# Kernel tuning notes

Measured on AMD Instinct MI355X. Metric: run time of the kernel, lower is better.

## Reference

```python
import jax, jax.numpy as jnp
import numpy as np

L, H, HS, D, T, V, B = 6, 6, 64, 384, 256, 65, 64
EPS = 1e-5


def layer_norm(x, g, b):
    m = x.mean(-1, keepdims=True)
    v = x.var(-1, keepdims=True)
    return (x - m) / jnp.sqrt(v + EPS) * g + b


def setup_inputs() -> dict:
    key = jax.random.key(0)
    ks = jax.random.split(key, 12)
    s = 0.02
    return {
        "idx": jax.random.randint(ks[0], (B, T), 0, V),
        "targets": jax.random.randint(ks[1], (B, T), 0, V),
        "tok_emb": s * jax.random.normal(ks[2], (V, D), jnp.float32),
        "pos_emb": s * jax.random.normal(ks[3], (T, D), jnp.float32),
        "Wq": s * jax.random.normal(ks[4], (L, H, D, HS), jnp.float32),
        "Wk": s * jax.random.normal(ks[5], (L, H, D, HS), jnp.float32),
        "Wv": s * jax.random.normal(ks[6], (L, H, D, HS), jnp.float32),
        "Wproj": s * jax.random.normal(ks[7], (L, D, D), jnp.float32),
        "bproj": jnp.zeros((L, D), jnp.float32),
        "W1": s * jax.random.normal(ks[8], (L, D, 4 * D), jnp.float32),
        "b1": jnp.zeros((L, 4 * D), jnp.float32),
        "W2": s * jax.random.normal(ks[9], (L, 4 * D, D), jnp.float32),
        "b2": jnp.zeros((L, D), jnp.float32),
        "ln1_g": jnp.ones((L, D), jnp.float32),
        "ln1_b": jnp.zeros((L, D), jnp.float32),
        "lnf_g": jnp.ones((D,), jnp.float32),
        "lnf_b": jnp.zeros((D,), jnp.float32),
        "Whead": s * jax.random.normal(ks[10], (D, V), jnp.float32),
        "bhead": jnp.zeros((V,), jnp.float32),
    }


def reference(idx, targets, tok_emb, pos_emb, Wq, Wk, Wv, Wproj, bproj,
              W1, b1, W2, b2, ln1_g, ln1_b, lnf_g, lnf_b, Whead, bhead):
    b, t = idx.shape
    x = tok_emb[idx] + pos_emb[:t]  # [B,T,D]
    mask = jnp.tril(jnp.ones((t, t), bool))
    scale = x.shape[-1] ** -0.5  # NOTE: original scales by n_emb_d**-0.5, not head_size**-0.5
    for l in range(L):
        y = layer_norm(x, ln1_g[l], ln1_b[l])
        q = jnp.einsum('btd,hde->bhte', y, Wq[l])
        k = jnp.einsum('btd,hde->bhte', y, Wk[l])
        v = jnp.einsum('btd,hde->bhte', y, Wv[l])
        w = jnp.einsum('bhte,bhse->bhts', q, k) * scale
        w = jnp.where(mask, w, -jnp.inf)
        w = jax.nn.softmax(w, axis=-1)
        o = jnp.einsum('bhts,bhse->bhte', w, v)
        o = o.transpose(0, 2, 1, 3).reshape(b, t, H * HS)  # concat heads on last dim
        x = x + o @ Wproj[l] + bproj[l]
        # NOTE: original Block reuses ln1 (not ln2) before the FFN -- replicated faithfully
        y2 = layer_norm(x, ln1_g[l], ln1_b[l])
        x = x + jax.nn.relu(y2 @ W1[l] + b1[l]) @ W2[l] + b2[l]
    x = layer_norm(x, lnf_g, lnf_b)
    logits = x @ Whead + bhead  # [B,T,V]
    logp = jax.nn.log_softmax(logits, axis=-1)
    loss = -jnp.take_along_axis(logp, targets[..., None], axis=-1).mean()
    return logits, loss
```

## Files before the change

### kernel.cpp

```cpp
#include <hip/hip_runtime.h>
#include <math.h>

#define L_ 6
#define H_ 6
#define HS_ 64
#define D_ 384
#define T_ 256
#define V_ 65
#define B_ 64
#define ROWS (B_*T_)
#define QKVN 1152
#define EPS_ 1e-5f

typedef __attribute__((ext_vector_type(8))) __bf16 bf16x8;
typedef __attribute__((ext_vector_type(4))) float f32x4;

__device__ __forceinline__ bf16x8 u4_to_bf8(uint4 u) {
    return __builtin_bit_cast(bf16x8, u);
}

__device__ __forceinline__ void glds16(const void* g, void* l) {
    __builtin_amdgcn_global_load_lds(
        (const __attribute__((address_space(1))) void*)g,
        (__attribute__((address_space(3))) void*)l, 16, 0, 0);
}

__global__ void embed_kernel(const int* __restrict__ idx,
                             const float* __restrict__ tok,
                             const float* __restrict__ pos,
                             float* __restrict__ x) {
    int i = blockIdx.x * blockDim.x + threadIdx.x;
    int d = i % D_;
    int row = i / D_;
    int t = row % T_;
    x[i] = tok[idx[row]*D_ + d] + pos[t*D_ + d];
}

__global__ __launch_bounds__(256)
void ln4(const float* __restrict__ x,
         const float* __restrict__ g,
         const float* __restrict__ b,
         __bf16* __restrict__ yb) {
    int w = threadIdx.x >> 6, lane = threadIdx.x & 63;
    int row = blockIdx.x * 4 + w;
    const float* xr = x + (size_t)row * D_;
    float v[6];
    #pragma unroll
    for (int i = 0; i < 6; ++i) v[i] = xr[lane + 64*i];
    float s = 0.f, sq = 0.f;
    #pragma unroll
    for (int i = 0; i < 6; ++i) { s += v[i]; sq += v[i]*v[i]; }
    for (int off = 32; off; off >>= 1) {
        s  += __shfl_xor(s,  off);
        sq += __shfl_xor(sq, off);
    }
    float mean = s * (1.0f/D_);
    float var  = sq * (1.0f/D_) - mean*mean;
    float rstd = rsqrtf(var + EPS_);
    __bf16* yr = yb + (size_t)row * D_;
    #pragma unroll
    for (int i = 0; i < 6; ++i) {
        int c = lane + 64*i;
        yr[c] = (__bf16)((v[i]-mean)*rstd*g[c] + b[c]);
    }
}

__global__ __launch_bounds__(256)
void transpose_cast(const float* __restrict__ src, __bf16* __restrict__ dst,
                    int R, int C, int zdiv, long sA, long sB, long dbase)
{
    __shared__ float tile[32][33];
    int z = blockIdx.z;
    const float* s = src + (long)z * R * C;
    __bf16* d = dst + dbase + (long)(z / zdiv) * sA + (long)(z % zdiv) * sB;
    int c0 = blockIdx.x * 32, r0 = blockIdx.y * 32;
    int t = threadIdx.x;
    int tr = t >> 3, tc = (t & 7) * 4;
    float4 v = *(const float4*)(s + (long)(r0 + tr) * C + c0 + tc);
    tile[tr][tc+0] = v.x; tile[tr][tc+1] = v.y;
    tile[tr][tc+2] = v.z; tile[tr][tc+3] = v.w;
    __syncthreads();
    #pragma unroll
    for (int j = 0; j < 4; ++j)
        d[(long)(c0 + tr) * R + r0 + tc + j] = (__bf16)tile[tc+j][tr];
}

__global__ __launch_bounds__(256)
void head_prep(const float* __restrict__ Whead, __bf16* __restrict__ headT) {
    int i = blockIdx.x * 256 + threadIdx.x;
    int n = i / D_, k = i % D_;
    headT[i] = (n < V_) ? (__bf16)Whead[k*V_ + n] : (__bf16)0.0f;
}

template<int TM>
__global__ __launch_bounds__(256)
void gemm_t(const __bf16* __restrict__ A, const __bf16* __restrict__ Bt,
            const float* __restrict__ bias, const float* res,
            float* outF, __bf16* outB,
            int K, int ldc, int ncols, int relu)
{
    constexpr int MI = TM / 32;
    __shared__ __align__(16) __bf16 As[2][TM*32];
    __shared__ __align__(16) __bf16 Bs[2][128*32];
    int t = threadIdx.x;
    int w = t >> 6, lane = t & 63;
    int ln = lane & 15, quad = lane >> 4;
    int n0 = blockIdx.x * 128, m0 = blockIdx.y * TM;
    int wm = (w >> 1) * (TM/2), wn = (w & 1) * 64;

    f32x4 acc[MI][4] = {};

    const char* Ab = (const char*)A + (size_t)m0 * K * 2;
    const char* Bb = (const char*)Bt + (size_t)n0 * K * 2;
    int f0 = w*64 + lane, f1 = f0 + 256;
    int r0 = f0 >> 2, r1 = f1 >> 2;
    size_t ga0 = (size_t)r0 * K * 2 + (size_t)(((f0 & 3) ^ (r0 & 3)) * 16);
    size_t ga1 = (size_t)r1 * K * 2 + (size_t)(((f1 & 3) ^ (r1 & 3)) * 16);
    int lo0 = w*64*16, lo1 = (w*64 + 256)*16;

    int nIt = K >> 5;
    glds16(Ab + ga0, (char*)As[0] + lo0);
    if constexpr (TM == 128) glds16(Ab + ga1, (char*)As[0] + lo1);
    glds16(Bb + ga0, (char*)Bs[0] + lo0);
    glds16(Bb + ga1, (char*)Bs[0] + lo1);

    for (int it = 0; it < nIt; ++it) {
        int p = it & 1;
        __syncthreads();
        if (it + 1 < nIt) {
            size_t kb = (size_t)(it + 1) * 64;
            glds16(Ab + ga0 + kb, (char*)As[p^1] + lo0);
            if constexpr (TM == 128) glds16(Ab + ga1 + kb, (char*)As[p^1] + lo1);
            glds16(Bb + ga0 + kb, (char*)Bs[p^1] + lo0);
            glds16(Bb + ga1 + kb, (char*)Bs[p^1] + lo1);
        }
        bf16x8 af[MI], bfr[4];
        #pragma unroll
        for (int i = 0; i < MI; ++i) {
            int row = wm + i*16 + ln;
            af[i] = __builtin_bit_cast(bf16x8,
                *(const uint4*)&As[p][row*32 + ((quad ^ (row & 3)) * 8)]);
        }
        #pragma unroll
        for (int j = 0; j < 4; ++j) {
            int row = wn + j*16 + ln;
            bfr[j] = __builtin_bit_cast(bf16x8,
                *(const uint4*)&Bs[p][row*32 + ((quad ^ (row & 3)) * 8)]);
        }
        #pragma unroll
        for (int i = 0; i < MI; ++i)
            #pragma unroll
            for (int j = 0; j < 4; ++j)
                acc[i][j] = __builtin_amdgcn_mfma_f32_16x16x32_bf16(
                                af[i], bfr[j], acc[i][j], 0, 0, 0);
        __syncthreads();
    }
    #pragma unroll
    for (int i = 0; i < MI; ++i) {
        #pragma unroll
        for (int r = 0; r < 4; ++r) {
            int row = m0 + wm + i*16 + quad*4 + r;
            #pragma unroll
            for (int j = 0; j < 4; ++j) {
                int col = n0 + wn + j*16 + ln;
                if (col < ncols) {
                    float v = acc[i][j][r];
                    if (bias) v += bias[col];
                    if (relu) v = fmaxf(v, 0.f);
                    if (res)  v += res[(size_t)row*ldc + col];
                    if (outF) outF[(size_t)row*ldc + col] = v;
                    if (outB) outB[(size_t)row*ldc + col] = (__bf16)v;
                }
            }
        }
    }
}

__global__ __launch_bounds__(256, 2)
void attn4(const __bf16* __restrict__ qkv, __bf16* __restrict__ o)
{
    __shared__ __align__(16) __bf16 Ks[256*72];
    __shared__ __align__(16) __bf16 Vt[64*264];
    __shared__ __align__(16) __bf16 Pw[4][32*40];
    int bid = blockIdx.x;
    int h = bid % H_;
    int b = bid / H_;
    int t = threadIdx.x;
    int w = t >> 6, lane = t & 63;
    int ln = lane & 15, quad = lane >> 4;
    const size_t rowb = (size_t)b * T_ * QKVN;
    const int hoff = h * HS_;
    const float scale = 0.05103103630798288f;

    for (int c = t; c < 2048; c += 256) {
        int r = c >> 3, e0 = (c & 7) * 8;
        uint4 uk = *(const uint4*)(qkv + rowb + (size_t)r*QKVN + 384 + hoff + e0);
        *(uint4*)&Ks[r*72 + e0] = uk;
        uint4 uv = *(const uint4*)(qkv + rowb + (size_t)r*QKVN + 768 + hoff + e0);
        bf16x8 v8 = u4_to_bf8(uv);
        #pragma unroll
        for (int j = 0; j < 8; ++j) {
            int e = e0 + j;
            Vt[e*264 + (((r >> 3) ^ ((e >> 3) & 3)) * 8) + (r & 7)] = v8[j];
        }
    }

    int qis[2] = { w, 7 - w };
    uint4 Qf[2][2][2];
    #pragma unroll
    for (int tl = 0; tl < 2; ++tl)
        #pragma unroll
        for (int mi = 0; mi < 2; ++mi)
            #pragma unroll
            for (int kc = 0; kc < 2; ++kc)
                Qf[tl][mi][kc] = *(const uint4*)(qkv + rowb +
                    (size_t)(qis[tl]*32 + mi*16 + ln)*QKVN + hoff + kc*32 + quad*8);

    __syncthreads();

    __bf16* P = Pw[w];
    #pragma unroll
    for (int tl = 0; tl < 2; ++tl) {
        int qi = qis[tl];
        f32x4 O[2][4] = {};
        float mst[2][4], lst[2][4];
        #pragma unroll
        for (int mi = 0; mi < 2; ++mi)
            #pragma unroll
            for (int r = 0; r < 4; ++r) { mst[mi][r] = -INFINITY; lst[mi][r] = 0.f; }

        for (int st = 0; st <= qi; ++st) {
            int sb = st * 32;
            f32x4 S[2][2] = {};
            #pragma unroll
            for (int kc = 0; kc < 2; ++kc) {
                uint4 Kf[2];
                #pragma unroll
                for (int ji = 0; ji < 2; ++ji)
                    Kf[ji] = *(const uint4*)&Ks[(sb + ji*16 + ln)*72 + kc*32 + quad*8];
                #pragma unroll
                for (int mi = 0; mi < 2; ++mi) {
                    bf16x8 qa = __builtin_bit_cast(bf16x8, Qf[tl][mi][kc]);
                    #pragma unroll
                    for (int ji = 0; ji < 2; ++ji)
                        S[mi][ji] = __builtin_amdgcn_mfma_f32_16x16x32_bf16(
                            qa, __builtin_bit_cast(bf16x8, Kf[ji]), S[mi][ji], 0, 0, 0);
                }
            }
            int diag = (st == qi);
            #pragma unroll
            for (int mi = 0; mi < 2; ++mi)
                #pragma unroll
                for (int ji = 0; ji < 2; ++ji)
                    #pragma unroll
                    for (int r = 0; r < 4; ++r) {
                        float v = S[mi][ji][r] * scale;
                        if (diag && (ji*16 + ln) > (mi*16 + quad*4 + r)) v = -INFINITY;
                        S[mi][ji][r] = v;
                    }
            #pragma unroll
            for (int mi = 0; mi < 2; ++mi)
                #pragma unroll
                for (int r = 0; r < 4; ++r) {
                    float mx = fmaxf(S[mi][0][r], S[mi][1][r]);
                    #pragma unroll
                    for (int off = 1; off < 16; off <<= 1)
                        mx = fmaxf(mx, __shfl_xor(mx, off));
                    float mn = fmaxf(mst[mi][r], mx);
                    float al = __expf(mst[mi][r] - mn);
                    mst[mi][r] = mn;
                    float p0 = __expf(S[mi][0][r] - mn);
                    float p1 = __expf(S[mi][1][r] - mn);
                    S[mi][0][r] = p0; S[mi][1][r] = p1;
                    float rs = p0 + p1;
                    #pragma unroll
                    for (int off = 1; off < 16; off <<= 1)
                        rs += __shfl_xor(rs, off);
                    lst[mi][r] = lst[mi][r]*al + rs;
                    #pragma unroll
                    for (int ei = 0; ei < 4; ++ei) O[mi][ei][r] *= al;
                }
            #pragma unroll
            for (int mi = 0; mi < 2; ++mi)
                #pragma unroll
                for (int ji = 0; ji < 2; ++ji)
                    #pragma unroll
                    for (int r = 0; r < 4; ++r)
                        P[(mi*16 + quad*4 + r)*40 + ji*16 + ln] = (__bf16)S[mi][ji][r];
            uint4 Pf[2], Vf[4];
            #pragma unroll
            for (int mi = 0; mi < 2; ++mi)
                Pf[mi] = *(const uint4*)&P[(mi*16 + ln)*40 + quad*8];
            #pragma unroll
            for (int ei = 0; ei < 4; ++ei) {
                int e = ei*16 + ln;
                Vf[ei] = *(const uint4*)&Vt[e*264 + (((st*4 + quad) ^ ((e >> 3) & 3)) * 8)];
            }
            #pragma unroll
            for (int mi = 0; mi < 2; ++mi)
                #pragma unroll
                for (int ei = 0; ei < 4; ++ei)
                    O[mi][ei] = __builtin_amdgcn_mfma_f32_16x16x32_bf16(
                        __builtin_bit_cast(bf16x8, Pf[mi]),
                        __builtin_bit_cast(bf16x8, Vf[ei]), O[mi][ei], 0, 0, 0);
        }
        #pragma unroll
        for (int mi = 0; mi < 2; ++mi)
            #pragma unroll
            for (int r = 0; r < 4; ++r) {
                float inv = 1.0f / lst[mi][r];
                size_t row = (size_t)(b*T_ + qi*32 + mi*16 + quad*4 + r);
                #pragma unroll
                for (int ei = 0; ei < 4; ++ei)
                    o[row*D_ + hoff + ei*16 + ln] = (__bf16)(O[mi][ei][r] * inv);
            }
    }
}

__global__ __launch_bounds__(256)
void loss2(const float* __restrict__ logits,
           const int* __restrict__ tg,
           float* __restrict__ loss)
{
    int row = blockIdx.x * 256 + threadIdx.x;
    const float* lr = logits + (size_t)row * V_;
    float m = -INFINITY;
    for (int c = 0; c < V_; ++c) m = fmaxf(m, lr[c]);
    float s = 0.f;
    for (int c = 0; c < V_; ++c) s += __expf(lr[c] - m);
    float val = -(lr[tg[row]] - m - __logf(s)) * (1.0f/ROWS);
    for (int off = 32; off; off >>= 1) val += __shfl_xor(val, off);
    __shared__ float red[4];
    int w = threadIdx.x >> 6, lane = threadIdx.x & 63;
    if (lane == 0) red[w] = val;
    __syncthreads();
    if (threadIdx.x == 0)
        atomicAdd(loss, red[0]+red[1]+red[2]+red[3]);
}

extern "C" void kernel_launch(void* const* d_in, const int* in_sizes, int n_in,
                              void* d_out, int out_size, void* d_ws, size_t ws_size,
                              hipStream_t stream)
{
    const int*   idx     = (const int*)  d_in[0];
    const int*   targets = (const int*)  d_in[1];
    const float* tok     = (const float*)d_in[2];
    const float* pos     = (const float*)d_in[3];
    const float* Wq      = (const float*)d_in[4];
    const float* Wk      = (const float*)d_in[5];
    const float* Wv      = (const float*)d_in[6];
    const float* Wproj   = (const float*)d_in[7];
    const float* bproj   = (const float*)d_in[8];
    const float* W1      = (const float*)d_in[9];
    const float* b1      = (const float*)d_in[10];
    const float* W2      = (const float*)d_in[11];
    const float* b2      = (const float*)d_in[12];
    const float* ln1g    = (const float*)d_in[13];
    const float* ln1b    = (const float*)d_in[14];
    const float* lnfg    = (const float*)d_in[15];
    const float* lnfb    = (const float*)d_in[16];
    const float* Whead   = (const float*)d_in[17];
    const float* bhead   = (const float*)d_in[18];

    float* logits = (float*)d_out;
    float* loss   = logits + (size_t)ROWS * V_;

    const size_t SZ = (size_t)ROWS * D_;
    const size_t RGELEMS = (size_t)ROWS * 4 * D_;

    float*  x   = (float*)d_ws;
    __bf16* yb  = (__bf16*)(x + SZ);
    __bf16* Rg  = yb + SZ;
    __bf16* qkv = Rg;
    __bf16* hid = Rg;
    __bf16* o   = Rg + RGELEMS;
    __bf16* qkvT  = o + SZ;
    __bf16* projT = qkvT + (size_t)L_*QKVN*D_;
    __bf16* w1T   = projT + (size_t)L_*D_*D_;
    __bf16* w2T   = w1T + (size_t)L_*D_*4*D_;
    __bf16* headT = w2T + (size_t)L_*D_*4*D_;

    transpose_cast<<<dim3(2,12,36),256,0,stream>>>(Wq, qkvT, D_, HS_, H_,
        (long)QKVN*D_, (long)HS_*D_, 0L);
    transpose_cast<<<dim3(2,12,36),256,0,stream>>>(Wk, qkvT, D_, HS_, H_,
        (long)QKVN*D_, (long)HS_*D_, (long)D_*D_);
    transpose_cast<<<dim3(2,12,36),256,0,stream>>>(Wv, qkvT, D_, HS_, H_,
        (long)QKVN*D_, (long)HS_*D_, 2L*D_*D_);
    transpose_cast<<<dim3(12,12,6),256,0,stream>>>(Wproj, projT, D_, D_, 1,
        (long)D_*D_, 0L, 0L);
    transpose_cast<<<dim3(48,12,6),256,0,stream>>>(W1, w1T, D_, 4*D_, 1,
        (long)D_*4*D_, 0L, 0L);
    transpose_cast<<<dim3(12,48,6),256,0,stream>>>(W2, w2T, 4*D_, D_, 1,
        (long)D_*4*D_, 0L, 0L);
    head_prep<<<(128*D_)/256, 256, 0, stream>>>(Whead, headT);

    embed_kernel<<<(ROWS*D_)/256, 256, 0, stream>>>(idx, tok, pos, x);

    for (int l = 0; l < L_; ++l) {
        ln4<<<ROWS/4, 256, 0, stream>>>(x, ln1g + l*D_, ln1b + l*D_, yb);
        gemm_t<128><<<dim3(QKVN/128, ROWS/128), 256, 0, stream>>>(
            yb, qkvT + (size_t)l*QKVN*D_, nullptr, nullptr, nullptr, qkv,
            D_, QKVN, QKVN, 0);
        attn4<<<B_*H_, 256, 0, stream>>>(qkv, o);
        gemm_t<64><<<dim3(D_/128, ROWS/64), 256, 0, stream>>>(
            o, projT + (size_t)l*D_*D_, bproj + l*D_, x, x, nullptr,
            D_, D_, D_, 0);
        ln4<<<ROWS/4, 256, 0, stream>>>(x, ln1g + l*D_, ln1b + l*D_, yb);
        gemm_t<128><<<dim3(4*D_/128, ROWS/128), 256, 0, stream>>>(
            yb, w1T + (size_t)l*D_*4*D_, b1 + l*4*D_, nullptr, nullptr, hid,
            D_, 4*D_, 4*D_, 1);
        gemm_t<64><<<dim3(D_/128, ROWS/64), 256, 0, stream>>>(
            hid, w2T + (size_t)l*D_*4*D_, b2 + l*D_, x, x, nullptr,
            4*D_, D_, D_, 0);
    }
    ln4<<<ROWS/4, 256, 0, stream>>>(x, lnfg, lnfb, yb);
    gemm_t<64><<<dim3(1, ROWS/64), 256, 0, stream>>>(
        yb, headT, bhead, nullptr, logits, nullptr,
        D_, V_, V_, 0);
    hipMemsetAsync(loss, 0, sizeof(float), stream);
    loss2<<<ROWS/256, 256, 0, stream>>>(logits, targets, loss);
}
```

Measured before the change: 1.529 ms.

## Store residual stream in bf16 and add K=96 single-stage GEMM for K=384

The residual stream x moves from fp32 to bf16. The layer norm, embedding and GEMM residual epilogues change to read and write bf16, which halves the traffic on the residual. A new gemm_k kernel loads 96-wide K chunks straight into LDS with a single buffer and is used for the K=384 GEMMs (QKV, proj, W1, head). Keeping the residual in bf16 loses precision that accumulates across layers and may push the output past tolerance. The new GEMM also gives up the double buffering the old kernel had.

```diff
diff --git a/kernel.cpp b/kernel.cpp
--- a/kernel.cpp
+++ b/kernel.cpp
@@ -28,25 +28,29 @@
 __global__ void embed_kernel(const int* __restrict__ idx,
                              const float* __restrict__ tok,
                              const float* __restrict__ pos,
-                             float* __restrict__ x) {
+                             __bf16* __restrict__ x) {
     int i = blockIdx.x * blockDim.x + threadIdx.x;
     int d = i % D_;
     int row = i / D_;
     int t = row % T_;
-    x[i] = tok[idx[row]*D_ + d] + pos[t*D_ + d];
+    x[i] = (__bf16)(tok[idx[row]*D_ + d] + pos[t*D_ + d]);
 }
 
 __global__ __launch_bounds__(256)
-void ln4(const float* __restrict__ x,
+void ln4(const __bf16* __restrict__ x,
          const float* __restrict__ g,
          const float* __restrict__ b,
          __bf16* __restrict__ yb) {
     int w = threadIdx.x >> 6, lane = threadIdx.x & 63;
     int row = blockIdx.x * 4 + w;
-    const float* xr = x + (size_t)row * D_;
+    const unsigned* xr = (const unsigned*)(x + (size_t)row * D_);
     float v[6];
     #pragma unroll
-    for (int i = 0; i < 6; ++i) v[i] = xr[lane + 64*i];
+    for (int i = 0; i < 3; ++i) {
+        unsigned u = xr[lane + 64*i];
+        v[2*i]   = __uint_as_float(u << 16);
+        v[2*i+1] = __uint_as_float(u & 0xffff0000u);
+    }
     float s = 0.f, sq = 0.f;
     #pragma unroll
     for (int i = 0; i < 6; ++i) { s += v[i]; sq += v[i]*v[i]; }
@@ -57,11 +61,15 @@
     float mean = s * (1.0f/D_);
     float var  = sq * (1.0f/D_) - mean*mean;
     float rstd = rsqrtf(var + EPS_);
-    __bf16* yr = yb + (size_t)row * D_;
-    #pragma unroll
-    for (int i = 0; i < 6; ++i) {
-        int c = lane + 64*i;
-        yr[c] = (__bf16)((v[i]-mean)*rstd*g[c] + b[c]);
+    unsigned* yr = (unsigned*)(yb + (size_t)row * D_);
+    #pragma unroll
+    for (int i = 0; i < 3; ++i) {
+        int c = 2*(lane + 64*i);
+        float o0 = (v[2*i]   - mean)*rstd*g[c]   + b[c];
+        float o1 = (v[2*i+1] - mean)*rstd*g[c+1] + b[c+1];
+        unsigned short h0 = __builtin_bit_cast(unsigned short, (__bf16)o0);
+        unsigned short h1 = __builtin_bit_cast(unsigned short, (__bf16)o1);
+        yr[lane + 64*i] = (unsigned)h0 | ((unsigned)h1 << 16);
     }
 }
 
@@ -94,8 +102,88 @@
 
 template<int TM>
 __global__ __launch_bounds__(256)
+void gemm_k(const __bf16* __restrict__ A, const __bf16* __restrict__ Bt,
+            const float* __restrict__ bias, const __bf16* res,
+            float* outF, __bf16* outB,
+            int K, int ldc, int ncols, int relu)
+{
+    constexpr int MI = TM / 32;
+    constexpr int AST = (TM*12)/256;
+    __shared__ __align__(16) __bf16 As[TM*96];
+    __shared__ __align__(16) __bf16 Bs[128*96];
+    int t = threadIdx.x;
+    int w = t >> 6, lane = t & 63;
+    int ln = lane & 15, quad = lane >> 4;
+    int n0 = blockIdx.x * 128, m0 = blockIdx.y * TM;
+    int wm = (w >> 1) * (TM/2), wn = (w & 1) * 64;
+
+    f32x4 acc[MI][4] = {};
+    const char* Ab = (const char*)A + (size_t)m0 * K * 2;
+    const char* Bb = (const char*)Bt + (size_t)n0 * K * 2;
+
+    int nIt = K / 96;
+    for (int it = 0; it < nIt; ++it) {
+        if (it) __syncthreads();
+        long kb = (long)it * 192;
+        #pragma unroll
+        for (int s = 0; s < AST; ++s) {
+            int c = s*256 + t;
+            int row = c / 12, ch = c - row*12;
+            glds16(Ab + (size_t)row*K*2 + kb + ch*16,
+                   (char*)As + (size_t)(s*256 + w*64)*16);
+        }
+        #pragma unroll
+        for (int s = 0; s < 6; ++s) {
+            int c = s*256 + t;
+            int row = c / 12, ch = c - row*12;
+            glds16(Bb + (size_t)row*K*2 + kb + ch*16,
+                   (char*)Bs + (size_t)(s*256 + w*64)*16);
+        }
+        __syncthreads();
+        #pragma unroll
+        for (int kk = 0; kk < 3; ++kk) {
+            bf16x8 af[MI], bfr[4];
+            #pragma unroll
+            for (int i = 0; i < MI; ++i)
+                af[i] = __builtin_bit_cast(bf16x8,
+                    *(const uint4*)&As[(wm + i*16 + ln)*96 + kk*32 + quad*8]);
+            #pragma unroll
+            for (int j = 0; j < 4; ++j)
+                bfr[j] = __builtin_bit_cast(bf16x8,
+                    *(const uint4*)&Bs[(wn + j*16 + ln)*96 + kk*32 + quad*8]);
+            #pragma unroll
+            for (int i = 0; i < MI; ++i)
+                #pragma unroll
+                for (int j = 0; j < 4; ++j)
+                    acc[i][j] = __builtin_amdgcn_mfma_f32_16x16x32_bf16(
+                                    af[i], bfr[j], acc[i][j], 0, 0, 0);
+        }
+    }
+    #pragma unroll
+    for (int i = 0; i < MI; ++i) {
+        #pragma unroll
+        for (int r = 0; r < 4; ++r) {
+            int row = m0 + wm + i*16 + quad*4 + r;
+            #pragma unroll
+            for (int j = 0; j < 4; ++j) {
+                int col = n0 + wn + j*16 + ln;
+                if (col < ncols) {
+                    float v = acc[i][j][r];
+                    if (bias) v += bias[col];
+                    if (relu) v = fmaxf(v, 0.f);
+                    if (res)  v += (float)res[(size_t)row*ldc + col];
+                    if (outF) outF[(size_t)row*ldc + col] = v;
+                    if (outB) outB[(size_t)row*ldc + col] = (__bf16)v;
+                }
+            }
+        }
+    }
+}
+
+template<int TM>
+__global__ __launch_bounds__(256)
 void gemm_t(const __bf16* __restrict__ A, const __bf16* __restrict__ Bt,
-            const float* __restrict__ bias, const float* res,
+            const float* __restrict__ bias, const __bf16* res,
             float* outF, __bf16* outB,
             int K, int ldc, int ncols, int relu)
 {
@@ -167,7 +255,7 @@
                     float v = acc[i][j][r];
                     if (bias) v += bias[col];
                     if (relu) v = fmaxf(v, 0.f);
-                    if (res)  v += res[(size_t)row*ldc + col];
+                    if (res)  v += (float)res[(size_t)row*ldc + col];
                     if (outF) outF[(size_t)row*ldc + col] = v;
                     if (outB) outB[(size_t)row*ldc + col] = (__bf16)v;
                 }
@@ -368,8 +456,8 @@
     const size_t SZ = (size_t)ROWS * D_;
     const size_t RGELEMS = (size_t)ROWS * 4 * D_;
 
-    float*  x   = (float*)d_ws;
-    __bf16* yb  = (__bf16*)(x + SZ);
+    __bf16* x   = (__bf16*)d_ws;
+    __bf16* yb  = x + SZ;
     __bf16* Rg  = yb + SZ;
     __bf16* qkv = Rg;
     __bf16* hid = Rg;
@@ -398,23 +486,23 @@
 
     for (int l = 0; l < L_; ++l) {
         ln4<<<ROWS/4, 256, 0, stream>>>(x, ln1g + l*D_, ln1b + l*D_, yb);
-        gemm_t<128><<<dim3(QKVN/128, ROWS/128), 256, 0, stream>>>(
+        gemm_k<128><<<dim3(QKVN/128, ROWS/128), 256, 0, stream>>>(
             yb, qkvT + (size_t)l*QKVN*D_, nullptr, nullptr, nullptr, qkv,
             D_, QKVN, QKVN, 0);
         attn4<<<B_*H_, 256, 0, stream>>>(qkv, o);
-        gemm_t<64><<<dim3(D_/128, ROWS/64), 256, 0, stream>>>(
-            o, projT + (size_t)l*D_*D_, bproj + l*D_, x, x, nullptr,
+        gemm_k<64><<<dim3(D_/128, ROWS/64), 256, 0, stream>>>(
+            o, projT + (size_t)l*D_*D_, bproj + l*D_, x, nullptr, x,
             D_, D_, D_, 0);
         ln4<<<ROWS/4, 256, 0, stream>>>(x, ln1g + l*D_, ln1b + l*D_, yb);
-        gemm_t<128><<<dim3(4*D_/128, ROWS/128), 256, 0, stream>>>(
+        gemm_k<128><<<dim3(4*D_/128, ROWS/128), 256, 0, stream>>>(
             yb, w1T + (size_t)l*D_*4*D_, b1 + l*4*D_, nullptr, nullptr, hid,
             D_, 4*D_, 4*D_, 1);
         gemm_t<64><<<dim3(D_/128, ROWS/64), 256, 0, stream>>>(
-            hid, w2T + (size_t)l*D_*4*D_, b2 + l*D_, x, x, nullptr,
+            hid, w2T + (size_t)l*D_*4*D_, b2 + l*D_, x, nullptr, x,
             4*D_, D_, D_, 0);
     }
     ln4<<<ROWS/4, 256, 0, stream>>>(x, lnfg, lnfb, yb);
-    gemm_t<64><<<dim3(1, ROWS/64), 256, 0, stream>>>(
+    gemm_k<64><<<dim3(1, ROWS/64), 256, 0, stream>>>(
         yb, headT, bhead, nullptr, logits, nullptr,
         D_, V_, V_, 0);
     hipMemsetAsync(loss, 0, sizeof(float), stream);
```

Result: slower. 1.610 ms (+5.3%).
